# Performance work log

Hardware: AMD Instinct MI355X
Metric: run time of the kernel (lower is better)

## Reference

```python
import jax, jax.numpy as jnp
import numpy as np


def setup_inputs() -> dict:
    key = jax.random.key(0)
    k0, k1, k2, k3, k4, k5 = jax.random.split(key, 6)
    B, S, D = 8, 4096, 1024
    x = jax.random.normal(k0, (B, S, D), dtype=jnp.float32)
    labels = jax.random.randint(k1, (B, S), 0, 2, dtype=jnp.int32)
    mask = jnp.ones((B, S), dtype=bool)  # torchcrf requires mask[:, 0] all on
    W = jax.random.normal(k2, (2, D), dtype=jnp.float32) / np.float32(np.sqrt(D))
    b = jnp.zeros((2,), dtype=jnp.float32)
    start_transitions = jax.random.uniform(k3, (2,), jnp.float32, -0.1, 0.1)
    end_transitions = jax.random.uniform(k4, (2,), jnp.float32, -0.1, 0.1)
    transitions = jax.random.uniform(k5, (2, 2), jnp.float32, -0.1, 0.1)
    return {"x": x, "labels": labels, "mask": mask, "W": W, "b": b,
            "start_transitions": start_transitions,
            "end_transitions": end_transitions,
            "transitions": transitions}


def _crf_neg_log_likelihood(logits, labels, mask, start_transitions, end_transitions, transitions):
    # torchcrf CRF(num_tags=2, batch_first=True), reduction='sum'
    maskf = mask.astype(logits.dtype)  # (B, S)
    # ---- numerator: score of the gold tag sequence ----
    emit = jnp.take_along_axis(logits, labels[..., None], axis=2)[..., 0]  # (B, S)
    num = start_transitions[labels[:, 0]] + emit[:, 0]
    num = num + jnp.sum(emit[:, 1:] * maskf[:, 1:], axis=1)
    num = num + jnp.sum(transitions[labels[:, :-1], labels[:, 1:]] * maskf[:, 1:], axis=1)
    seq_ends = jnp.sum(mask.astype(jnp.int32), axis=1) - 1  # (B,)
    last_tags = jnp.take_along_axis(labels, seq_ends[:, None], axis=1)[:, 0]
    num = num + end_transitions[last_tags]
    # ---- denominator: forward algorithm (log partition) via scan over time ----
    def step(alpha, inp):
        e, m = inp  # e: (B, 2) emissions at t, m: (B,) mask at t
        nxt = jax.nn.logsumexp(alpha[:, :, None] + transitions[None, :, :] + e[:, None, :], axis=1)
        alpha = jnp.where(m[:, None], nxt, alpha)
        return alpha, None
    alpha0 = start_transitions[None, :] + logits[:, 0]  # (B, 2)
    emis_t = jnp.swapaxes(logits, 0, 1)[1:]  # (S-1, B, 2)
    mask_t = jnp.swapaxes(mask, 0, 1)[1:]    # (S-1, B)
    alpha, _ = jax.lax.scan(step, alpha0, (emis_t, mask_t))
    logZ = jax.nn.logsumexp(alpha + end_transitions[None, :], axis=1)  # (B,)
    llh = jnp.sum(num - logZ)  # reduction='sum'
    return -llh


def reference(x, labels, mask, W, b, start_transitions, end_transitions, transitions):
    # dropout is identity at inference
    logits = jnp.einsum('bsd,td->bst', x, W) + b  # (B, S, 2)
    neg_llh = _crf_neg_log_likelihood(logits, labels, mask,
                                      start_transitions, end_transitions, transitions)
    # module returns (-loss, logits) where loss = crf(...) = log-likelihood sum
    return (neg_llh, logits)
```

## Files before the change

### kernel.cpp

```cpp
#include <hip/hip_runtime.h>
#include <math.h>

#define NB 8
#define S  4096
#define D  1024
#define RPW 4

__global__ __launch_bounds__(256, 4) void logits_kernel(
    const float* __restrict__ x, const float* __restrict__ W,
    const float* __restrict__ b, float* __restrict__ out)
{
    int wave = (blockIdx.x * blockDim.x + threadIdx.x) >> 6;
    int lane = threadIdx.x & 63;
    int row0 = wave * RPW;

    float4 w0[4], w1[4];
#pragma unroll
    for (int k = 0; k < 4; ++k) {
        int c = (lane + 64 * k) * 4;
        w0[k] = *(const float4*)(W + c);
        w1[k] = *(const float4*)(W + D + c);
    }
    float b0 = b[0], b1 = b[1];

#pragma unroll
    for (int r = 0; r < RPW; ++r) {
        const float* xr = x + (size_t)(row0 + r) * D;
        float4 xv[4];
#pragma unroll
        for (int k = 0; k < 4; ++k) xv[k] = *(const float4*)(xr + (lane + 64 * k) * 4);
        float a0 = 0.f, a1 = 0.f;
#pragma unroll
        for (int k = 0; k < 4; ++k) {
            a0 += xv[k].x*w0[k].x + xv[k].y*w0[k].y + xv[k].z*w0[k].z + xv[k].w*w0[k].w;
            a1 += xv[k].x*w1[k].x + xv[k].y*w1[k].y + xv[k].z*w1[k].z + xv[k].w*w1[k].w;
        }
#pragma unroll
        for (int off = 32; off >= 1; off >>= 1) {
            a0 += __shfl_xor(a0, off, 64);
            a1 += __shfl_xor(a1, off, 64);
        }
        if (lane == 0) {
            size_t o = 1 + (size_t)(row0 + r) * 2;
            out[o]     = a0 + b0;
            out[o + 1] = a1 + b1;
        }
    }
    if (blockIdx.x == 0 && threadIdx.x == 0) out[0] = 0.f;
}

__device__ inline float lse2(float a, float b) {
    float m = fmaxf(a, b);
    float d = fminf(a, b) - m;
    return m + __logf(1.f + __expf(d));
}

__global__ __launch_bounds__(256) void crf_kernel(
    const float* __restrict__ out_logits,
    const int*   __restrict__ labels,
    const float* __restrict__ start_t,
    const float* __restrict__ end_t,
    const float* __restrict__ trans,
    float* __restrict__ result)
{
    const int bidx = blockIdx.x;
    const int t = threadIdx.x;
    const float* lg  = out_logits + 1 + (size_t)bidx * S * 2;
    const int*   lab = labels + (size_t)bidx * S;
    const float tr00 = trans[0], tr01 = trans[1], tr10 = trans[2], tr11 = trans[3];

    int cstart = 1 + t * 16;
    int cend   = min(cstart + 16, S);
    float e0 = lg[cstart*2+0], e1 = lg[cstart*2+1];
    float P00 = tr00 + e0, P01 = tr01 + e1, P10 = tr10 + e0, P11 = tr11 + e1;
    for (int s = cstart + 1; s < cend; ++s) {
        e0 = lg[s*2+0]; e1 = lg[s*2+1];
        float M00 = tr00+e0, M01 = tr01+e1, M10 = tr10+e0, M11 = tr11+e1;
        float n00 = lse2(P00+M00, P01+M10);
        float n01 = lse2(P00+M01, P01+M11);
        float n10 = lse2(P10+M00, P11+M10);
        float n11 = lse2(P10+M01, P11+M11);
        P00=n00; P01=n01; P10=n10; P11=n11;
    }

    __shared__ float4 Ps[256];
    Ps[t] = make_float4(P00, P01, P10, P11);
    __syncthreads();
    for (int off = 1; off < 256; off <<= 1) {
        if ((t & (2*off - 1)) == 0) {
            float4 A = Ps[t], B = Ps[t + off];
            float4 R;
            R.x = lse2(A.x + B.x, A.y + B.z);
            R.y = lse2(A.x + B.y, A.y + B.w);
            R.z = lse2(A.z + B.x, A.w + B.z);
            R.w = lse2(A.z + B.y, A.w + B.w);
            Ps[t] = R;
        }
        __syncthreads();
    }

    float acc = 0.f;
    for (int s = t; s < S; s += 256) {
        int l = lab[s];
        acc += lg[s*2 + l];
        if (s >= 1) acc += trans[lab[s-1]*2 + l];
    }
    __shared__ float red[256];
    red[t] = acc;
    __syncthreads();
    for (int off = 128; off >= 1; off >>= 1) {
        if (t < off) red[t] += red[t + off];
        __syncthreads();
    }

    if (t == 0) {
        float4 P = Ps[0];
        float a0 = start_t[0] + lg[0];
        float a1 = start_t[1] + lg[1];
        float f0 = lse2(a0 + P.x, a1 + P.z);
        float f1 = lse2(a0 + P.y, a1 + P.w);
        float logZ = lse2(f0 + end_t[0], f1 + end_t[1]);
        float num  = start_t[lab[0]] + red[0] + end_t[lab[S-1]];
        atomicAdd(result, logZ - num);
    }
}

extern "C" void kernel_launch(void* const* d_in, const int* in_sizes, int n_in,
                              void* d_out, int out_size, void* d_ws, size_t ws_size,
                              hipStream_t stream) {
    const float* x      = (const float*)d_in[0];
    const int*   labels = (const int*)  d_in[1];
    const float* W      = (const float*)d_in[3];
    const float* b      = (const float*)d_in[4];
    const float* st     = (const float*)d_in[5];
    const float* et     = (const float*)d_in[6];
    const float* tr     = (const float*)d_in[7];
    float* out = (float*)d_out;

    const int waves  = NB * S / RPW;
    const int blocks = waves / 4;
    logits_kernel<<<blocks, 256, 0, stream>>>(x, W, b, out);
    crf_kernel<<<NB, 256, 0, stream>>>(out, labels, st, et, tr, out);
}
```

Baseline: 224.6 us.

## Fuse per-wave CRF transfer matrices and gold scores into logits kernel

```diff
diff --git a/kernel.cpp b/kernel.cpp
--- a/kernel.cpp
+++ b/kernel.cpp
@@ -5,14 +5,27 @@
 #define S  4096
 #define D  1024
 #define RPW 4
+#define NWAVES (NB * S / RPW)
+
+__device__ inline float lse2(float a, float b) {
+    float m = fmaxf(a, b);
+    float d = fminf(a, b) - m;
+    return m + __logf(1.f + __expf(d));
+}
 
 __global__ __launch_bounds__(256, 4) void logits_kernel(
     const float* __restrict__ x, const float* __restrict__ W,
-    const float* __restrict__ b, float* __restrict__ out)
+    const float* __restrict__ b, const int* __restrict__ labels,
+    const float* __restrict__ trans,
+    float* __restrict__ out,
+    float4* __restrict__ wsP,
+    float* __restrict__ wsN)
 {
     int wave = (blockIdx.x * blockDim.x + threadIdx.x) >> 6;
     int lane = threadIdx.x & 63;
     int row0 = wave * RPW;
+    int s0   = row0 & (S - 1);
+    int batch = row0 >> 12;
 
     float4 w0[4], w1[4];
 #pragma unroll
@@ -22,7 +35,13 @@
         w1[k] = *(const float4*)(W + D + c);
     }
     float b0 = b[0], b1 = b[1];
+    float tr00 = trans[0], tr01 = trans[1], tr10 = trans[2], tr11 = trans[3];
 
+    const int* labp = labels + batch * S + s0;
+    int lm1 = (s0 > 0) ? labp[-1] : 0;
+    int l0 = labp[0], l1 = labp[1], l2 = labp[2], l3 = labp[3];
+
+    float2 ee[4];
 #pragma unroll
     for (int r = 0; r < RPW; ++r) {
         const float* xr = x + (size_t)(row0 + r) * D;
@@ -40,88 +59,104 @@
             a0 += __shfl_xor(a0, off, 64);
             a1 += __shfl_xor(a1, off, 64);
         }
+        ee[r].x = a0 + b0;
+        ee[r].y = a1 + b1;
         if (lane == 0) {
             size_t o = 1 + (size_t)(row0 + r) * 2;
-            out[o]     = a0 + b0;
-            out[o + 1] = a1 + b1;
+            out[o]     = ee[r].x;
+            out[o + 1] = ee[r].y;
         }
+    }
+
+    auto trsel = [&](int i, int j) {
+        return j ? (i ? tr11 : tr01) : (i ? tr10 : tr00);
+    };
+    float num = (l0 ? ee[0].y : ee[0].x)
+              + (l1 ? ee[1].y : ee[1].x)
+              + (l2 ? ee[2].y : ee[2].x)
+              + (l3 ? ee[3].y : ee[3].x);
+    num += trsel(l0, l1) + trsel(l1, l2) + trsel(l2, l3);
+    if (s0 > 0) num += trsel(lm1, l0);
+
+    float P00, P01, P10, P11;
+    auto comb = [&](float2 e) {
+        float M00 = tr00 + e.x, M01 = tr01 + e.y, M10 = tr10 + e.x, M11 = tr11 + e.y;
+        float n00 = lse2(P00 + M00, P01 + M10);
+        float n01 = lse2(P00 + M01, P01 + M11);
+        float n10 = lse2(P10 + M00, P11 + M10);
+        float n11 = lse2(P10 + M01, P11 + M11);
+        P00 = n00; P01 = n01; P10 = n10; P11 = n11;
+    };
+    if (s0 == 0) {
+        P00 = tr00 + ee[1].x; P01 = tr01 + ee[1].y;
+        P10 = tr10 + ee[1].x; P11 = tr11 + ee[1].y;
+        comb(ee[2]); comb(ee[3]);
+    } else {
+        P00 = tr00 + ee[0].x; P01 = tr01 + ee[0].y;
+        P10 = tr10 + ee[0].x; P11 = tr11 + ee[0].y;
+        comb(ee[1]); comb(ee[2]); comb(ee[3]);
+    }
+
+    if (lane == 0) {
+        wsP[wave] = make_float4(P00, P01, P10, P11);
+        wsN[wave] = num;
     }
     if (blockIdx.x == 0 && threadIdx.x == 0) out[0] = 0.f;
 }
 
-__device__ inline float lse2(float a, float b) {
-    float m = fmaxf(a, b);
-    float d = fminf(a, b) - m;
-    return m + __logf(1.f + __expf(d));
-}
-
-__global__ __launch_bounds__(256) void crf_kernel(
-    const float* __restrict__ out_logits,
-    const int*   __restrict__ labels,
-    const float* __restrict__ start_t,
-    const float* __restrict__ end_t,
-    const float* __restrict__ trans,
+__global__ __launch_bounds__(256) void crf_reduce_kernel(
+    const float* __restrict__ out_logits, const int* __restrict__ labels,
+    const float* __restrict__ start_t, const float* __restrict__ end_t,
+    const float4* __restrict__ wsP, const float* __restrict__ wsN,
     float* __restrict__ result)
 {
     const int bidx = blockIdx.x;
     const int t = threadIdx.x;
-    const float* lg  = out_logits + 1 + (size_t)bidx * S * 2;
-    const int*   lab = labels + (size_t)bidx * S;
-    const float tr00 = trans[0], tr01 = trans[1], tr10 = trans[2], tr11 = trans[3];
+    const int wbase = bidx * (S / RPW) + t * 4;
 
-    int cstart = 1 + t * 16;
-    int cend   = min(cstart + 16, S);
-    float e0 = lg[cstart*2+0], e1 = lg[cstart*2+1];
-    float P00 = tr00 + e0, P01 = tr01 + e1, P10 = tr10 + e0, P11 = tr11 + e1;
-    for (int s = cstart + 1; s < cend; ++s) {
-        e0 = lg[s*2+0]; e1 = lg[s*2+1];
-        float M00 = tr00+e0, M01 = tr01+e1, M10 = tr10+e0, M11 = tr11+e1;
-        float n00 = lse2(P00+M00, P01+M10);
-        float n01 = lse2(P00+M01, P01+M11);
-        float n10 = lse2(P10+M00, P11+M10);
-        float n11 = lse2(P10+M01, P11+M11);
-        P00=n00; P01=n01; P10=n10; P11=n11;
+    float4 A = wsP[wbase];
+    float num = wsN[wbase];
+#pragma unroll
+    for (int k = 1; k < 4; ++k) {
+        float4 Bm = wsP[wbase + k];
+        num += wsN[wbase + k];
+        float4 R;
+        R.x = lse2(A.x + Bm.x, A.y + Bm.z);
+        R.y = lse2(A.x + Bm.y, A.y + Bm.w);
+        R.z = lse2(A.z + Bm.x, A.w + Bm.z);
+        R.w = lse2(A.z + Bm.y, A.w + Bm.w);
+        A = R;
     }
 
     __shared__ float4 Ps[256];
-    Ps[t] = make_float4(P00, P01, P10, P11);
+    __shared__ float red[256];
+    Ps[t] = A; red[t] = num;
     __syncthreads();
     for (int off = 1; off < 256; off <<= 1) {
-        if ((t & (2*off - 1)) == 0) {
-            float4 A = Ps[t], B = Ps[t + off];
+        if ((t & (2 * off - 1)) == 0) {
+            float4 Aa = Ps[t], Bb = Ps[t + off];
             float4 R;
-            R.x = lse2(A.x + B.x, A.y + B.z);
-            R.y = lse2(A.x + B.y, A.y + B.w);
-            R.z = lse2(A.z + B.x, A.w + B.z);
-            R.w = lse2(A.z + B.y, A.w + B.w);
+            R.x = lse2(Aa.x + Bb.x, Aa.y + Bb.z);
+            R.y = lse2(Aa.x + Bb.y, Aa.y + Bb.w);
+            R.z = lse2(Aa.z + Bb.x, Aa.w + Bb.z);
+            R.w = lse2(Aa.z + Bb.y, Aa.w + Bb.w);
             Ps[t] = R;
+            red[t] += red[t + off];
         }
         __syncthreads();
     }
 
-    float acc = 0.f;
-    for (int s = t; s < S; s += 256) {
-        int l = lab[s];
-        acc += lg[s*2 + l];
-        if (s >= 1) acc += trans[lab[s-1]*2 + l];
-    }
-    __shared__ float red[256];
-    red[t] = acc;
-    __syncthreads();
-    for (int off = 128; off >= 1; off >>= 1) {
-        if (t < off) red[t] += red[t + off];
-        __syncthreads();
-    }
-
     if (t == 0) {
+        const float* lg  = out_logits + 1 + (size_t)bidx * S * 2;
+        const int*   lab = labels + (size_t)bidx * S;
         float4 P = Ps[0];
         float a0 = start_t[0] + lg[0];
         float a1 = start_t[1] + lg[1];
         float f0 = lse2(a0 + P.x, a1 + P.z);
         float f1 = lse2(a0 + P.y, a1 + P.w);
         float logZ = lse2(f0 + end_t[0], f1 + end_t[1]);
-        float num  = start_t[lab[0]] + red[0] + end_t[lab[S-1]];
-        atomicAdd(result, logZ - num);
+        float numt = red[0] + start_t[lab[0]] + end_t[lab[S - 1]];
+        atomicAdd(result, logZ - numt);
     }
 }
 
@@ -137,8 +172,11 @@
     const float* tr     = (const float*)d_in[7];
     float* out = (float*)d_out;
 
+    float4* wsP = (float4*)d_ws;
+    float*  wsN = (float*)((char*)d_ws + (size_t)NWAVES * sizeof(float4));
+
     const int waves  = NB * S / RPW;
     const int blocks = waves / 4;
-    logits_kernel<<<blocks, 256, 0, stream>>>(x, W, b, out);
-    crf_kernel<<<NB, 256, 0, stream>>>(out, labels, st, et, tr, out);
+    logits_kernel<<<blocks, 256, 0, stream>>>(x, W, b, labels, tr, out, wsP, wsN);
+    crf_reduce_kernel<<<NB, 256, 0, stream>>>(out, labels, st, et, wsP, wsN, out);
 }
```

Measured after the change: 214.4 us. 1.05x faster.
